# Kernel tuning notes

Measured on AMD Instinct MI355X. Metric: run time of the kernel, lower is better.

The kernel has to match this reference:

```python
import jax, jax.numpy as jnp
import numpy as np

B, NCH, NT = 64, 129, 200
D_MODEL, D_STATE, D_CONV, HEADDIM, NLAYERS = 256, 16, 4, 32, 4
D_INNER = 2 * D_MODEL            # expand=2 -> 512
NHEADS = D_INNER // HEADDIM      # 16
CONV_DIM = D_INNER + 2 * D_STATE # 544 (ngroups=1)
D_IN_PROJ = 2 * D_INNER + 2 * D_STATE + NHEADS  # 1072


def silu(x):
    return x * jax.nn.sigmoid(x)


def layernorm(x, w, b, eps=1e-5):
    m = x.mean(-1, keepdims=True)
    v = ((x - m) ** 2).mean(-1, keepdims=True)
    return (x - m) * jax.lax.rsqrt(v + eps) * w + b


def dwconv(x, w, b, pad):
    # x: (B, C, T), w: (C, K) depthwise, pad: (left, right)
    y = jax.lax.conv_general_dilated(x, w[:, None, :], (1,), [pad],
                                     feature_group_count=x.shape[1])
    return y + b[None, :, None]


def mamba2_block(u, Wi, cw, cb, dtb, Alog, Dh, nw, Wo):
    # u: (b, l, d_model)
    b, l, _ = u.shape
    zxbcdt = u @ Wi.T  # (b, l, 1072)
    z, xBC, dt = jnp.split(zxbcdt, [D_INNER, D_INNER + CONV_DIM], axis=-1)
    dt = jax.nn.softplus(dt + dtb)  # (b, l, nheads)
    # causal depthwise conv + silu on xBC
    xBC = silu(dwconv(xBC.transpose(0, 2, 1), cw, cb, (D_CONV - 1, 0)).transpose(0, 2, 1))
    xh, Bm, Cm = jnp.split(xBC, [D_INNER, D_INNER + D_STATE], axis=-1)
    xh = xh.reshape(b, l, NHEADS, HEADDIM)
    A = -jnp.exp(Alog)              # (h,)
    dA = jnp.exp(dt * A)            # (b, l, h)
    dtx = dt[..., None] * xh        # (b, l, h, p)

    def step(hst, inp):
        dA_t, dtx_t, B_t, C_t = inp
        hst = dA_t[:, :, None, None] * hst + dtx_t[..., None] * B_t[:, None, None, :]
        y_t = jnp.einsum('bhpn,bn->bhp', hst, C_t)
        return hst, y_t

    h0 = jnp.zeros((b, NHEADS, HEADDIM, D_STATE), u.dtype)
    _, ys = jax.lax.scan(step, h0, (dA.swapaxes(0, 1), dtx.swapaxes(0, 1),
                                    Bm.swapaxes(0, 1), Cm.swapaxes(0, 1)))
    y = ys.swapaxes(0, 1) + xh * Dh[None, None, :, None]  # (b, l, h, p)
    y = y.reshape(b, l, D_INNER)
    # gated RMSNorm (norm_before_gate=False): gate first, then rmsnorm
    y = y * silu(z)
    y = y * jax.lax.rsqrt((y * y).mean(-1, keepdims=True) + 1e-5) * nw
    return y @ Wo.T


def setup_inputs() -> dict:
    key = jax.random.key(0)
    ks = iter(jax.random.split(key, 32))
    nrm = lambda shape, s=0.02: jax.random.normal(next(ks), shape, jnp.float32) * s
    dt0 = jax.random.uniform(next(ks), (NLAYERS, NHEADS), minval=1e-3, maxval=0.1)
    return {
        'x': jax.random.normal(next(ks), (B, NCH, NT), jnp.float32),
        'emb': nrm((NCH, D_MODEL), 1.0),
        'sconv_w': nrm((NCH, 3), 0.3),
        'sconv_b': jnp.zeros((NCH,), jnp.float32),
        'mixer_w': nrm((D_MODEL, NCH), 0.05),
        'mixer_b': jnp.zeros((D_MODEL,), jnp.float32),
        'enc_ln_w': jnp.ones((D_MODEL,), jnp.float32),
        'enc_ln_b': jnp.zeros((D_MODEL,), jnp.float32),
        'in_proj_w': nrm((NLAYERS, D_IN_PROJ, D_MODEL)),
        'conv_w': nrm((NLAYERS, CONV_DIM, D_CONV), 0.3),
        'conv_b': jnp.zeros((NLAYERS, CONV_DIM), jnp.float32),
        'dt_bias': jnp.log(jnp.expm1(dt0)),
        'A_log': jnp.log(jax.random.uniform(next(ks), (NLAYERS, NHEADS), minval=1.0, maxval=16.0)),
        'D_skip': jnp.ones((NLAYERS, NHEADS), jnp.float32),
        'norm_w': jnp.ones((NLAYERS, D_INNER), jnp.float32),
        'out_proj_w': nrm((NLAYERS, D_MODEL, D_INNER)),
        'ln_w': jnp.ones((NLAYERS, D_MODEL), jnp.float32),
        'ln_b': jnp.zeros((NLAYERS, D_MODEL), jnp.float32),
        'head1_w': nrm((D_MODEL // 2, D_MODEL), 0.05),
        'head1_b': jnp.zeros((D_MODEL // 2,), jnp.float32),
        'head2_w': nrm((1, D_MODEL // 2), 0.05),
        'head2_b': jnp.zeros((1,), jnp.float32),
    }


def reference(x, emb, sconv_w, sconv_b, mixer_w, mixer_b, enc_ln_w, enc_ln_b,
              in_proj_w, conv_w, conv_b, dt_bias, A_log, D_skip, norm_w,
              out_proj_w, ln_w, ln_b, head1_w, head1_b, head2_w, head2_b):
    # SpatialChannelEncoder: depthwise conv over time + channel-mixing Linear
    xs = dwconv(x, sconv_w, sconv_b, (1, 1))                  # (b, c, t)
    h = jnp.einsum('bct,dc->btd', xs, mixer_w) + mixer_b      # (b, t, d)
    h = h + emb.mean(0)                                       # mean channel embedding
    h = layernorm(h, enc_ln_w, enc_ln_b)                      # dropout=identity (eval)
    # Stacked Mamba2 blocks with post-norm residual
    for i in range(NLAYERS):
        res = h
        y = mamba2_block(h, in_proj_w[i], conv_w[i], conv_b[i], dt_bias[i],
                         A_log[i], D_skip[i], norm_w[i], out_proj_w[i])
        h = layernorm(y + res, ln_w[i], ln_b[i])
    pooled = h.mean(1)                                        # AdaptiveAvgPool1d(1)
    hid = jax.nn.relu(pooled @ head1_w.T + head1_b)
    return hid @ head2_w.T + head2_b                          # (b, 1)
```

## Files before the change

### kernel.cpp

```cpp
#include <hip/hip_runtime.h>
#include <math.h>

#define B_   64
#define T_   200
#define DM   256
#define DI   512
#define NH   16
#define HD   32
#define DSZ  16
#define CD   544
#define DIP  1072
#define M_TOT (B_*T_)
#define NCH_ 129
#define KENC 192
#define NCHUNK 10
#define CLEN  20
#define NBC  48

typedef unsigned short u16;
typedef unsigned int u32;
typedef _Float16 f16;
typedef __attribute__((ext_vector_type(8))) _Float16 half8;
typedef __attribute__((ext_vector_type(4))) short short4v;
typedef __attribute__((ext_vector_type(4))) float f32x4;

__device__ __forceinline__ float wave_sum(float v) {
    #pragma unroll
    for (int off = 32; off > 0; off >>= 1) v += __shfl_xor(v, off);
    return v;
}
__device__ __forceinline__ void split_f16(float a, u16& hi, u16& lo) {
    f16 h = (f16)a;
    f16 l = (f16)(a - (float)h);
    hi = __builtin_bit_cast(u16, h);
    lo = __builtin_bit_cast(u16, l);
}
__device__ __forceinline__ u16 f16bits(float a) {
    f16 h = (f16)a;
    return __builtin_bit_cast(u16, h);
}

__global__ void emb_mean_k(const float* __restrict__ emb, float* __restrict__ em) {
    int d = threadIdx.x;
    float s = 0.f;
    for (int c = 0; c < NCH_; ++c) s += emb[c * DM + d];
    em[d] = s * (1.f / NCH_);
}

__global__ void xsA2_k(const float* __restrict__ x, const float* __restrict__ w,
                       const float* __restrict__ b, u16* __restrict__ A2) {
    int idx = blockIdx.x * blockDim.x + threadIdx.x;
    if (idx >= M_TOT * KENC) return;
    int c = idx % KENC;
    int m = idx / KENC;
    float acc = 0.f;
    if (c < NCH_) {
        int t = m % T_;
        int bb = m / T_;
        const float* xr = x + (size_t)(bb * NCH_ + c) * T_;
        acc = b[c];
        if (t > 0)      acc += w[c*3+0] * xr[t-1];
        acc += w[c*3+1] * xr[t];
        if (t < T_-1)   acc += w[c*3+2] * xr[t+1];
    }
    u16 hi, lo; split_f16(acc, hi, lo);
    u16* row = A2 + (size_t)m * (2*KENC);
    row[c] = hi; row[KENC + c] = lo;
}

__global__ void pack_b2_k(const float* __restrict__ W, u16* __restrict__ B2,
                          int L, int N, int Npad, int Kreal, int K) {
    int idx = blockIdx.x * blockDim.x + threadIdx.x;
    if (idx >= L * Npad * K) return;
    int k = idx % K;
    int n = (idx / K) % Npad;
    int l = idx / (K * Npad);
    u16 hi = 0;
    if (n < N && k < Kreal)
        hi = f16bits(W[((size_t)l * N + n) * Kreal + k]);
    u16* row = B2 + ((size_t)l * Npad + n) * 2 * K;
    row[k] = hi;
    row[K + k] = hi;
}

__global__ __launch_bounds__(256) void gemm_m64n128(const u16* __restrict__ A2,
                                                    const u16* __restrict__ B2,
                                                    float* __restrict__ C,
                                                    int K2, int ldc, int Nreal,
                                                    int nbx) {
    __shared__ u16 As[64 * 64];
    __shared__ u16 Bs[128 * 64];
    int nwg = gridDim.x;
    int lin = blockIdx.x;
    int q = nwg >> 3, r = nwg & 7;
    int xcd = lin & 7, idx = lin >> 3;
    int wg = ((xcd < r) ? xcd * (q + 1) : r * (q + 1) + (xcd - r) * q) + idx;
    int bx = wg % nbx, by = wg / nbx;

    int tid = threadIdx.x;
    int lane = tid & 63;
    int wave = tid >> 6;
    int wr = wave >> 1;
    int wc = wave & 1;
    int bm = by * 64;
    int bn = bx * 128;

    f32x4 acc[2][4] = {};
    const size_t ldA = (size_t)K2 * 2;

    for (int k0 = 0; k0 < K2; k0 += 64) {
        #pragma unroll
        for (int c = 0; c < 2; ++c) {
            int o = c * 4096 + tid * 16;
            int row = o >> 7;
            int slot = (o >> 4) & 7;
            int ss = slot ^ (row & 7);
            const char* src = (const char*)A2 + (size_t)(bm + row) * ldA
                              + (size_t)k0 * 2 + ss * 16;
            __builtin_amdgcn_global_load_lds(
                (const __attribute__((address_space(1))) u32*)src,
                (__attribute__((address_space(3))) u32*)((char*)As + o),
                16, 0, 0);
        }
        #pragma unroll
        for (int c = 0; c < 4; ++c) {
            int o = c * 4096 + tid * 16;
            int row = o >> 7;
            int slot = (o >> 4) & 7;
            int ss = slot ^ (row & 7);
            const char* src = (const char*)B2 + (size_t)(bn + row) * ldA
                              + (size_t)k0 * 2 + ss * 16;
            __builtin_amdgcn_global_load_lds(
                (const __attribute__((address_space(1))) u32*)src,
                (__attribute__((address_space(3))) u32*)((char*)Bs + o),
                16, 0, 0);
        }
        __syncthreads();
        #pragma unroll
        for (int kk = 0; kk < 2; ++kk) {
            int lslot = kk * 4 + (lane >> 4);
            half8 afr[2], bfr[4];
            #pragma unroll
            for (int n = 0; n < 4; ++n) {
                int row = wc * 64 + n * 16 + (lane & 15);
                int ps = lslot ^ (row & 7);
                bfr[n] = *(const half8*)((const char*)Bs + row * 128 + ps * 16);
            }
            #pragma unroll
            for (int m = 0; m < 2; ++m) {
                int row = wr * 32 + m * 16 + (lane & 15);
                int ps = lslot ^ (row & 7);
                afr[m] = *(const half8*)((const char*)As + row * 128 + ps * 16);
            }
            #pragma unroll
            for (int m = 0; m < 2; ++m)
                #pragma unroll
                for (int n = 0; n < 4; ++n)
                    acc[m][n] = __builtin_amdgcn_mfma_f32_16x16x32_f16(
                        bfr[n], afr[m], acc[m][n], 0, 0, 0);
        }
        __syncthreads();
    }

    int crow0 = bm + wr * 32;
    int ccol0 = bn + wc * 64;
    #pragma unroll
    for (int m = 0; m < 2; ++m) {
        int row = crow0 + m * 16 + (lane & 15);
        #pragma unroll
        for (int n = 0; n < 4; ++n) {
            int col = ccol0 + n * 16 + (lane >> 4) * 4;
            if (col < Nreal)
                *(f32x4*)(C + (size_t)row * ldc + col) = acc[m][n];
        }
    }
}

__global__ __launch_bounds__(256) void gemm_m64n64(const u16* __restrict__ A2,
                                                   const u16* __restrict__ B2,
                                                   float* __restrict__ C,
                                                   int K2, int ldc, int Nreal,
                                                   int nbx) {
    __shared__ u16 As[64 * 64];
    __shared__ u16 Bs[64 * 64];
    int nwg = gridDim.x;
    int lin = blockIdx.x;
    int q = nwg >> 3, r = nwg & 7;
    int xcd = lin & 7, idx = lin >> 3;
    int wg = ((xcd < r) ? xcd * (q + 1) : r * (q + 1) + (xcd - r) * q) + idx;
    int bx = wg % nbx, by = wg / nbx;

    int tid = threadIdx.x;
    int lane = tid & 63;
    int wave = tid >> 6;
    int wr = wave >> 1;
    int wc = wave & 1;
    int bm = by * 64;
    int bn = bx * 64;

    f32x4 acc[2][2] = {};
    const size_t ldA = (size_t)K2 * 2;

    for (int k0 = 0; k0 < K2; k0 += 64) {
        #pragma unroll
        for (int c = 0; c < 2; ++c) {
            int o = c * 4096 + tid * 16;
            int row = o >> 7;
            int slot = (o >> 4) & 7;
            int ss = slot ^ (row & 7);
            const char* src = (const char*)A2 + (size_t)(bm + row) * ldA
                              + (size_t)k0 * 2 + ss * 16;
            __builtin_amdgcn_global_load_lds(
                (const __attribute__((address_space(1))) u32*)src,
                (__attribute__((address_space(3))) u32*)((char*)As + o),
                16, 0, 0);
        }
        #pragma unroll
        for (int c = 0; c < 2; ++c) {
            int o = c * 4096 + tid * 16;
            int row = o >> 7;
            int slot = (o >> 4) & 7;
            int ss = slot ^ (row & 7);
            const char* src = (const char*)B2 + (size_t)(bn + row) * ldA
                              + (size_t)k0 * 2 + ss * 16;
            __builtin_amdgcn_global_load_lds(
                (const __attribute__((address_space(1))) u32*)src,
                (__attribute__((address_space(3))) u32*)((char*)Bs + o),
                16, 0, 0);
        }
        __syncthreads();
        #pragma unroll
        for (int kk = 0; kk < 2; ++kk) {
            int lslot = kk * 4 + (lane >> 4);
            half8 afr[2], bfr[2];
            #pragma unroll
            for (int n = 0; n < 2; ++n) {
                int row = wc * 32 + n * 16 + (lane & 15);
                int ps = lslot ^ (row & 7);
                bfr[n] = *(const half8*)((const char*)Bs + row * 128 + ps * 16);
            }
            #pragma unroll
            for (int m = 0; m < 2; ++m) {
                int row = wr * 32 + m * 16 + (lane & 15);
                int ps = lslot ^ (row & 7);
                afr[m] = *(const half8*)((const char*)As + row * 128 + ps * 16);
            }
            #pragma unroll
            for (int m = 0; m < 2; ++m)
                #pragma unroll
                for (int n = 0; n < 2; ++n)
                    acc[m][n] = __builtin_amdgcn_mfma_f32_16x16x32_f16(
                        bfr[n], afr[m], acc[m][n], 0, 0, 0);
        }
        __syncthreads();
    }

    int crow0 = bm + wr * 32;
    int ccol0 = bn + wc * 32;
    #pragma unroll
    for (int m = 0; m < 2; ++m) {
        int row = crow0 + m * 16 + (lane & 15);
        #pragma unroll
        for (int n = 0; n < 2; ++n) {
            int col = ccol0 + n * 16 + (lane >> 4) * 4;
            if (col < Nreal)
                *(f32x4*)(C + (size_t)row * ldc + col) = acc[m][n];
        }
    }
}

__global__ __launch_bounds__(256) void enc_ln_k(float* __restrict__ h,
        const float* __restrict__ mb, const float* __restrict__ em,
        const float* __restrict__ w, const float* __restrict__ bb,
        u16* __restrict__ A2) {
    int row = blockIdx.x * 4 + (threadIdx.x >> 6);
    int lane = threadIdx.x & 63;
    int e = lane * 4;
    float* hr = h + (size_t)row * DM;
    f32x4 v = *(const f32x4*)(hr + e);
    f32x4 vm = *(const f32x4*)(mb + e);
    f32x4 ve = *(const f32x4*)(em + e);
    float s = 0.f, sq = 0.f;
    #pragma unroll
    for (int j = 0; j < 4; ++j) {
        v[j] += vm[j] + ve[j];
        s += v[j];
        sq += v[j] * v[j];
    }
    s = wave_sum(s); sq = wave_sum(sq);
    float mean = s * (1.f / DM);
    float var = sq * (1.f / DM) - mean * mean;
    float r = rsqrtf(var + 1e-5f);
    f32x4 vw = *(const f32x4*)(w + e);
    f32x4 vb = *(const f32x4*)(bb + e);
    f32x4 o;
    short4v hi4, lo4;
    #pragma unroll
    for (int j = 0; j < 4; ++j) {
        float ov = (v[j] - mean) * r * vw[j] + vb[j];
        o[j] = ov;
        u16 hi, lo; split_f16(ov, hi, lo);
        hi4[j] = (short)hi; lo4[j] = (short)lo;
    }
    *(f32x4*)(hr + e) = o;
    u16* ar = A2 + (size_t)row * 512;
    *(short4v*)(ar + e) = hi4;
    *(short4v*)(ar + 256 + e) = lo4;
}

__global__ void bc_dt_k(const float* __restrict__ zx, const float* __restrict__ cw,
                        const float* __restrict__ cb, const float* __restrict__ dtb_in,
                        const float* __restrict__ A_log,
                        float* __restrict__ xbcs, float* __restrict__ dtb,
                        float* __restrict__ dAb) {
    int idx = blockIdx.x * blockDim.x + threadIdx.x;
    if (idx >= M_TOT * NBC) return;
    int c = idx % NBC;
    int m = idx / NBC;
    if (c < 32) {
        int cc = 512 + c;
        int t = m % T_;
        float acc = cb[cc];
        #pragma unroll
        for (int k = 0; k < 4; ++k) {
            int tt = t - 3 + k;
            if (tt >= 0) acc += cw[cc*4+k] * zx[(size_t)(m - (3 - k)) * DIP + DI + cc];
        }
        xbcs[(size_t)m * NBC + c] = acc / (1.f + expf(-acc));
    } else {
        int h = c - 32;
        float xv = zx[(size_t)m * DIP + DI + CD + h] + dtb_in[h];
        float dt = (xv > 20.f) ? xv : log1pf(expf(xv));
        float A = -expf(A_log[h]);
        dtb[m * NH + h] = dt;
        dAb[m * NH + h] = expf(dt * A);
    }
}

__global__ __launch_bounds__(128) void scan1_k(const float* __restrict__ zx,
        const float* __restrict__ xbcs, const float* __restrict__ dtb,
        const float* __restrict__ dAb, const float* __restrict__ cw,
        const float* __restrict__ cb, const float* __restrict__ D_skip,
        float* __restrict__ y, float* __restrict__ S, float* __restrict__ Pprod) {
    int c   = blockIdx.x % NCHUNK;
    int bhq = blockIdx.x / NCHUNK;
    int b   = bhq >> 2;
    int hq  = bhq & 3;
    int h   = hq * 4 + (threadIdx.x >> 5);
    int p   = threadIdx.x & 31;
    int ch  = h * HD + p;
    float Dh = D_skip[h];
    float w0 = cw[ch*4+0], w1 = cw[ch*4+1], w2 = cw[ch*4+2], w3 = cw[ch*4+3];
    float cbb = cb[ch];
    float s[16];
    #pragma unroll
    for (int n = 0; n < 16; ++n) s[n] = 0.f;
    float pr = 1.f;
    int t0 = c * CLEN;
    int base = b * T_ + t0;
    const float* xsrc = zx + (size_t)base * DIP + DI + ch;
    float xm3 = (t0 >= 3) ? xsrc[-3 * (ptrdiff_t)DIP] : 0.f;
    float xm2 = (t0 >= 2) ? xsrc[-2 * (ptrdiff_t)DIP] : 0.f;
    float xm1 = (t0 >= 1) ? xsrc[-1 * (ptrdiff_t)DIP] : 0.f;
    float x0  = xsrc[0];
    float dt = dtb[base * NH + h];
    float dA = dAb[base * NH + h];
    const float* bcr = xbcs + (size_t)base * NBC;
    f32x4 Bv[4], Cv[4];
    #pragma unroll
    for (int qq = 0; qq < 4; ++qq) {
        Bv[qq] = *(const f32x4*)(bcr + qq * 4);
        Cv[qq] = *(const f32x4*)(bcr + 16 + qq * 4);
    }
    for (int t = 0; t < CLEN; ++t) {
        int m = base + t;
        int tn = (t + 1 < CLEN) ? t + 1 : t;
        float x0n  = xsrc[(size_t)tn * DIP];
        float dt_n = dtb[(base + tn) * NH + h];
        float dA_n = dAb[(base + tn) * NH + h];
        const float* bcn = xbcs + (size_t)(base + tn) * NBC;
        f32x4 Bn_[4], Cn_[4];
        #pragma unroll
        for (int qq = 0; qq < 4; ++qq) {
            Bn_[qq] = *(const f32x4*)(bcn + qq * 4);
            Cn_[qq] = *(const f32x4*)(bcn + 16 + qq * 4);
        }
        float a = cbb + w0 * xm3 + w1 * xm2 + w2 * xm1 + w3 * x0;
        float xh = a / (1.f + expf(-a));
        pr *= dA;
        float dtx = dt * xh;
        float ya0 = 0.f, ya1 = 0.f, ya2 = 0.f, ya3 = 0.f;
        #pragma unroll
        for (int qq = 0; qq < 4; ++qq) {
            #pragma unroll
            for (int j = 0; j < 4; ++j) {
                int n = qq * 4 + j;
                s[n] = fmaf(dA, s[n], dtx * Bv[qq][j]);
                float prod = s[n] * Cv[qq][j];
                if (qq == 0) ya0 += prod;
                else if (qq == 1) ya1 += prod;
                else if (qq == 2) ya2 += prod;
                else ya3 += prod;
            }
        }
        y[(size_t)m * DI + ch] = fmaf(Dh, xh, (ya0 + ya1) + (ya2 + ya3));
        xm3 = xm2; xm2 = xm1; xm1 = x0; x0 = x0n;
        dt = dt_n; dA = dA_n;
        #pragma unroll
        for (int qq = 0; qq < 4; ++qq) { Bv[qq] = Bn_[qq]; Cv[qq] = Cn_[qq]; }
    }
    size_t sidx = ((((size_t)b * NH + h) * NCHUNK + c) * 32 + p) * 16;
    #pragma unroll
    for (int qq = 0; qq < 4; ++qq) {
        f32x4 v; v[0]=s[qq*4]; v[1]=s[qq*4+1]; v[2]=s[qq*4+2]; v[3]=s[qq*4+3];
        *(f32x4*)(S + sidx + qq * 4) = v;
    }
    if (p == 0) Pprod[(b * NH + h) * NCHUNK + c] = pr;
}

__global__ __launch_bounds__(128) void scan2_k(float* __restrict__ S,
        const float* __restrict__ Pprod) {
    int b  = blockIdx.x >> 2;
    int hq = blockIdx.x & 3;
    int h  = hq * 4 + (threadIdx.x >> 5);
    int p  = threadIdx.x & 31;
    float s[16];
    #pragma unroll
    for (int n = 0; n < 16; ++n) s[n] = 0.f;
    size_t bh = (size_t)b * NH + h;
    for (int c = 1; c < NCHUNK; ++c) {
        float P = Pprod[bh * NCHUNK + (c - 1)];
        size_t eidx = ((bh * NCHUNK + (c - 1)) * 32 + p) * 16;
        #pragma unroll
        for (int qq = 0; qq < 4; ++qq) {
            f32x4 e = *(const f32x4*)(S + eidx + qq * 4);
            f32x4 o;
            #pragma unroll
            for (int j = 0; j < 4; ++j) {
                s[qq*4+j] = fmaf(P, s[qq*4+j], e[j]);
                o[j] = s[qq*4+j];
            }
            *(f32x4*)(S + eidx + qq * 4) = o;
        }
    }
}

__global__ __launch_bounds__(128) void scan3_k(const float* __restrict__ xbcs,
        const float* __restrict__ dAb, const float* __restrict__ S,
        float* __restrict__ y) {
    int c   = (blockIdx.x % (NCHUNK - 1)) + 1;
    int bhq = blockIdx.x / (NCHUNK - 1);
    int b   = bhq >> 2;
    int hq  = bhq & 3;
    int h   = hq * 4 + (threadIdx.x >> 5);
    int p   = threadIdx.x & 31;
    size_t iidx = ((((size_t)b * NH + h) * NCHUNK + (c - 1)) * 32 + p) * 16;
    float si[16];
    #pragma unroll
    for (int qq = 0; qq < 4; ++qq) {
        f32x4 v = *(const f32x4*)(S + iidx + qq * 4);
        si[qq*4] = v[0]; si[qq*4+1] = v[1]; si[qq*4+2] = v[2]; si[qq*4+3] = v[3];
    }
    float cum = 1.f;
    int base = b * T_ + c * CLEN;
    for (int t = 0; t < CLEN; ++t) {
        int m = base + t;
        cum *= dAb[m * NH + h];
        const float* Cr = xbcs + (size_t)m * NBC + 16;
        float dot = 0.f;
        #pragma unroll
        for (int qq = 0; qq < 4; ++qq) {
            f32x4 Cv = *(const f32x4*)(Cr + qq * 4);
            #pragma unroll
            for (int j = 0; j < 4; ++j) dot = fmaf(si[qq*4+j], Cv[j], dot);
        }
        y[(size_t)m * DI + h * HD + p] += cum * dot;
    }
}

__global__ __launch_bounds__(256) void gate_rms_k(const float* __restrict__ y,
        const float* __restrict__ zx, const float* __restrict__ nw,
        u16* __restrict__ A2) {
    int row = blockIdx.x * 4 + (threadIdx.x >> 6);
    int lane = threadIdx.x & 63;
    int e0 = lane * 4, e1 = 256 + lane * 4;
    const float* yr = y + (size_t)row * DI;
    const float* zr = zx + (size_t)row * DIP;
    f32x4 y0 = *(const f32x4*)(yr + e0);
    f32x4 y1 = *(const f32x4*)(yr + e1);
    f32x4 z0 = *(const f32x4*)(zr + e0);
    f32x4 z1 = *(const f32x4*)(zr + e1);
    f32x4 g0, g1;
    float sq = 0.f;
    #pragma unroll
    for (int j = 0; j < 4; ++j) {
        g0[j] = y0[j] * (z0[j] / (1.f + expf(-z0[j])));
        g1[j] = y1[j] * (z1[j] / (1.f + expf(-z1[j])));
        sq += g0[j] * g0[j] + g1[j] * g1[j];
    }
    sq = wave_sum(sq);
    float r = rsqrtf(sq * (1.f / DI) + 1e-5f);
    f32x4 w0 = *(const f32x4*)(nw + e0);
    f32x4 w1 = *(const f32x4*)(nw + e1);
    u16* ar = A2 + (size_t)row * 1024;
    short4v hi4, lo4;
    #pragma unroll
    for (int j = 0; j < 4; ++j) {
        float ov = g0[j] * r * w0[j];
        u16 hi, lo; split_f16(ov, hi, lo);
        hi4[j] = (short)hi; lo4[j] = (short)lo;
    }
    *(short4v*)(ar + e0) = hi4;
    *(short4v*)(ar + 512 + e0) = lo4;
    #pragma unroll
    for (int j = 0; j < 4; ++j) {
        float ov = g1[j] * r * w1[j];
        u16 hi, lo; split_f16(ov, hi, lo);
        hi4[j] = (short)hi; lo4[j] = (short)lo;
    }
    *(short4v*)(ar + e1) = hi4;
    *(short4v*)(ar + 512 + e1) = lo4;
}

__global__ __launch_bounds__(256) void add_ln_k(float* __restrict__ h,
        const float* __restrict__ c, const float* __restrict__ w,
        const float* __restrict__ bb, u16* __restrict__ A2) {
    int row = blockIdx.x * 4 + (threadIdx.x >> 6);
    int lane = threadIdx.x & 63;
    int e = lane * 4;
    float* hr = h + (size_t)row * DM;
    const float* cr = c + (size_t)row * DM;
    f32x4 v = *(const f32x4*)(hr + e);
    f32x4 vc = *(const f32x4*)(cr + e);
    float s = 0.f, sq = 0.f;
    #pragma unroll
    for (int j = 0; j < 4; ++j) {
        v[j] += vc[j];
        s += v[j];
        sq += v[j] * v[j];
    }
    s = wave_sum(s); sq = wave_sum(sq);
    float mean = s * (1.f / DM);
    float var = sq * (1.f / DM) - mean * mean;
    float r = rsqrtf(var + 1e-5f);
    f32x4 vw = *(const f32x4*)(w + e);
    f32x4 vb = *(const f32x4*)(bb + e);
    f32x4 o;
    short4v hi4, lo4;
    #pragma unroll
    for (int j = 0; j < 4; ++j) {
        float ov = (v[j] - mean) * r * vw[j] + vb[j];
        o[j] = ov;
        u16 hi, lo; split_f16(ov, hi, lo);
        hi4[j] = (short)hi; lo4[j] = (short)lo;
    }
    *(f32x4*)(hr + e) = o;
    u16* ar = A2 + (size_t)row * 512;
    *(short4v*)(ar + e) = hi4;
    *(short4v*)(ar + 256 + e) = lo4;
}

__global__ __launch_bounds__(256) void pool_head_k(const float* __restrict__ h,
        const float* __restrict__ w1, const float* __restrict__ b1,
        const float* __restrict__ w2, const float* __restrict__ b2,
        float* __restrict__ out) {
    __shared__ float pl[DM];
    __shared__ float red[2];
    int b = blockIdx.x, tid = threadIdx.x;
    float s = 0.f;
    for (int t = 0; t < T_; ++t) s += h[(size_t)(b * T_ + t) * DM + tid];
    pl[tid] = s * (1.f / T_);
    __syncthreads();
    float v = 0.f;
    if (tid < 128) {
        float acc = b1[tid];
        #pragma unroll 4
        for (int d = 0; d < DM; ++d) acc = fmaf(pl[d], w1[tid * DM + d], acc);
        v = fmaxf(acc, 0.f) * w2[tid];
    }
    #pragma unroll
    for (int off = 32; off > 0; off >>= 1) v += __shfl_xor(v, off);
    if (tid == 0) red[0] = v;
    if (tid == 64) red[1] = v;
    __syncthreads();
    if (tid == 0) out[b] = red[0] + red[1] + b2[0];
}

extern "C" void kernel_launch(void* const* d_in, const int* in_sizes, int n_in,
                              void* d_out, int out_size, void* d_ws, size_t ws_size,
                              hipStream_t stream) {
    const float* x         = (const float*)d_in[0];
    const float* emb       = (const float*)d_in[1];
    const float* sconv_w   = (const float*)d_in[2];
    const float* sconv_b   = (const float*)d_in[3];
    const float* mixer_w   = (const float*)d_in[4];
    const float* mixer_b   = (const float*)d_in[5];
    const float* enc_ln_w  = (const float*)d_in[6];
    const float* enc_ln_b  = (const float*)d_in[7];
    const float* in_proj_w = (const float*)d_in[8];
    const float* conv_w    = (const float*)d_in[9];
    const float* conv_b    = (const float*)d_in[10];
    const float* dt_bias   = (const float*)d_in[11];
    const float* A_log     = (const float*)d_in[12];
    const float* D_skip    = (const float*)d_in[13];
    const float* norm_w    = (const float*)d_in[14];
    const float* out_proj_w= (const float*)d_in[15];
    const float* ln_w      = (const float*)d_in[16];
    const float* ln_b      = (const float*)d_in[17];
    const float* head1_w   = (const float*)d_in[18];
    const float* head1_b   = (const float*)d_in[19];
    const float* head2_w   = (const float*)d_in[20];
    const float* head2_b   = (const float*)d_in[21];
    float* out = (float*)d_out;

    float* ws  = (float*)d_ws;
    float* h    = ws;
    float* zx   = h    + (size_t)M_TOT * DM;
    float* xbcs = zx   + (size_t)M_TOT * DIP;
    float* y    = xbcs + (size_t)M_TOT * NBC;
    float* dtb  = y    + (size_t)M_TOT * DI;
    float* dAb  = dtb  + (size_t)M_TOT * NH;
    float* em   = dAb  + (size_t)M_TOT * NH;
    float* scrap = em + 256;
    u16* A2  = (u16*)scrap;
    u16* B2e = A2 + (size_t)12800 * 1024;
    u16* B2i = B2e + (size_t)256 * 384;
    u16* B2o = B2i + (size_t)4 * 1152 * 512;

    float* S     = (float*)A2;
    float* Pprod = S + (size_t)B_*NH*NCHUNK*512;

    emb_mean_k<<<1, DM, 0, stream>>>(emb, em);
    pack_b2_k<<<(256 * KENC + 255) / 256, 256, 0, stream>>>(
        mixer_w, B2e, 1, DM, DM, NCH_, KENC);
    pack_b2_k<<<(4 * 1152 * DM + 255) / 256, 256, 0, stream>>>(
        in_proj_w, B2i, 4, DIP, 1152, DM, DM);
    pack_b2_k<<<(4 * 256 * DI + 255) / 256, 256, 0, stream>>>(
        out_proj_w, B2o, 4, DM, DM, DI, DI);

    xsA2_k<<<(M_TOT * KENC + 255) / 256, 256, 0, stream>>>(x, sconv_w, sconv_b, A2);
    gemm_m64n64<<<4 * 200, 256, 0, stream>>>(A2, B2e, h, 2 * KENC, DM, DM, 4);
    enc_ln_k<<<M_TOT / 4, 256, 0, stream>>>(h, mixer_b, em, enc_ln_w, enc_ln_b, A2);

    for (int l = 0; l < 4; ++l) {
        gemm_m64n128<<<9 * 200, 256, 0, stream>>>(
            A2, B2i + (size_t)l * 1152 * 512, zx, 512, DIP, DIP, 9);

        bc_dt_k<<<(M_TOT * NBC + 255) / 256, 256, 0, stream>>>(
            zx, conv_w + l * CD * 4, conv_b + l * CD, dt_bias + l * NH,
            A_log + l * NH, xbcs, dtb, dAb);

        scan1_k<<<B_ * 4 * NCHUNK, 128, 0, stream>>>(
            zx, xbcs, dtb, dAb, conv_w + l * CD * 4, conv_b + l * CD,
            D_skip + l * NH, y, S, Pprod);
        scan2_k<<<B_ * 4, 128, 0, stream>>>(S, Pprod);
        scan3_k<<<B_ * 4 * (NCHUNK - 1), 128, 0, stream>>>(xbcs, dAb, S, y);

        gate_rms_k<<<M_TOT / 4, 256, 0, stream>>>(y, zx, norm_w + l * DI, A2);

        gemm_m64n64<<<4 * 200, 256, 0, stream>>>(
            A2, B2o + (size_t)l * 256 * 1024, zx, 1024, DM, DM, 4);

        add_ln_k<<<M_TOT / 4, 256, 0, stream>>>(h, zx, ln_w + l * DM, ln_b + l * DM, A2);
    }

    pool_head_k<<<B_, 256, 0, stream>>>(h, head1_w, head1_b, head2_w, head2_b, out);
}
```

Baseline: 575.8 us.

## Fold inter-chunk state propagation into scan3 and drop scan2 kernel

Removes the separate sequential inter-chunk state pass (scan2) and instead has each scan3 block rebuild its incoming state directly as a weighted sum of the end states of all earlier chunks, weighted by cumulative decay products. This removes one kernel launch and the serial per-(batch,head) pass that wrote states back to memory, in exchange for redundant reads of earlier chunk states (quadratic in chunk count, up to nine chunks). The floating-point summation order changes slightly.

Measured after the change: 583.4 us. About the same (+1.3%).

```diff
diff --git a/kernel.cpp b/kernel.cpp
--- a/kernel.cpp
+++ b/kernel.cpp
@@ -418,48 +418,30 @@
     if (p == 0) Pprod[(b * NH + h) * NCHUNK + c] = pr;
 }
 
-__global__ __launch_bounds__(128) void scan2_k(float* __restrict__ S,
-        const float* __restrict__ Pprod) {
-    int b  = blockIdx.x >> 2;
-    int hq = blockIdx.x & 3;
-    int h  = hq * 4 + (threadIdx.x >> 5);
-    int p  = threadIdx.x & 31;
-    float s[16];
-    #pragma unroll
-    for (int n = 0; n < 16; ++n) s[n] = 0.f;
-    size_t bh = (size_t)b * NH + h;
-    for (int c = 1; c < NCHUNK; ++c) {
-        float P = Pprod[bh * NCHUNK + (c - 1)];
-        size_t eidx = ((bh * NCHUNK + (c - 1)) * 32 + p) * 16;
-        #pragma unroll
-        for (int qq = 0; qq < 4; ++qq) {
-            f32x4 e = *(const f32x4*)(S + eidx + qq * 4);
-            f32x4 o;
-            #pragma unroll
-            for (int j = 0; j < 4; ++j) {
-                s[qq*4+j] = fmaf(P, s[qq*4+j], e[j]);
-                o[j] = s[qq*4+j];
-            }
-            *(f32x4*)(S + eidx + qq * 4) = o;
-        }
-    }
-}
-
 __global__ __launch_bounds__(128) void scan3_k(const float* __restrict__ xbcs,
         const float* __restrict__ dAb, const float* __restrict__ S,
-        float* __restrict__ y) {
+        const float* __restrict__ Pprod, float* __restrict__ y) {
     int c   = (blockIdx.x % (NCHUNK - 1)) + 1;
     int bhq = blockIdx.x / (NCHUNK - 1);
     int b   = bhq >> 2;
     int hq  = bhq & 3;
     int h   = hq * 4 + (threadIdx.x >> 5);
     int p   = threadIdx.x & 31;
-    size_t iidx = ((((size_t)b * NH + h) * NCHUNK + (c - 1)) * 32 + p) * 16;
+    size_t bh = (size_t)b * NH + h;
     float si[16];
     #pragma unroll
-    for (int qq = 0; qq < 4; ++qq) {
-        f32x4 v = *(const f32x4*)(S + iidx + qq * 4);
-        si[qq*4] = v[0]; si[qq*4+1] = v[1]; si[qq*4+2] = v[2]; si[qq*4+3] = v[3];
+    for (int n = 0; n < 16; ++n) si[n] = 0.f;
+    float wgt = 1.f;
+    for (int j = c - 1; j >= 0; --j) {
+        size_t eidx = ((bh * NCHUNK + j) * 32 + p) * 16;
+        #pragma unroll
+        for (int qq = 0; qq < 4; ++qq) {
+            f32x4 e = *(const f32x4*)(S + eidx + qq * 4);
+            #pragma unroll
+            for (int jj = 0; jj < 4; ++jj)
+                si[qq*4+jj] = fmaf(wgt, e[jj], si[qq*4+jj]);
+        }
+        wgt *= Pprod[bh * NCHUNK + j];
     }
     float cum = 1.f;
     int base = b * T_ + c * CLEN;
@@ -472,7 +454,7 @@
         for (int qq = 0; qq < 4; ++qq) {
             f32x4 Cv = *(const f32x4*)(Cr + qq * 4);
             #pragma unroll
-            for (int j = 0; j < 4; ++j) dot = fmaf(si[qq*4+j], Cv[j], dot);
+            for (int jj = 0; jj < 4; ++jj) dot = fmaf(si[qq*4+jj], Cv[jj], dot);
         }
         y[(size_t)m * DI + h * HD + p] += cum * dot;
     }
@@ -653,8 +635,7 @@
         scan1_k<<<B_ * 4 * NCHUNK, 128, 0, stream>>>(
             zx, xbcs, dtb, dAb, conv_w + l * CD * 4, conv_b + l * CD,
             D_skip + l * NH, y, S, Pprod);
-        scan2_k<<<B_ * 4, 128, 0, stream>>>(S, Pprod);
-        scan3_k<<<B_ * 4 * (NCHUNK - 1), 128, 0, stream>>>(xbcs, dAb, S, y);
+        scan3_k<<<B_ * 4 * (NCHUNK - 1), 128, 0, stream>>>(xbcs, dAb, S, Pprod, y);
 
         gate_rms_k<<<M_TOT / 4, 256, 0, stream>>>(y, zx, norm_w + l * DI, A2);
 
```
